# Kernel optimization log

Hardware: AMD Instinct MI355X
Metric: run time of the kernel (lower is better)

## Reference

```python
import jax, jax.numpy as jnp
import numpy as np

B, T, M, S = 16384, 128, 4, 12  # num_series, timesteps, measurements, states


def setup_inputs() -> dict:
    key = jax.random.key(0)
    ks = jax.random.split(key, 7)
    inp = jax.random.normal(ks[0], (B, T, M), dtype=jnp.float32)
    # stable transition matrix near identity
    F = jnp.eye(S, dtype=jnp.float32) + 0.05 * jax.random.normal(ks[1], (S, S), dtype=jnp.float32) / np.float32(np.sqrt(S))
    H = jax.random.normal(ks[2], (M, S), dtype=jnp.float32) / np.float32(np.sqrt(S))
    Aq = 0.1 * jax.random.normal(ks[3], (S, S), dtype=jnp.float32)
    Q = Aq @ Aq.T + 1e-3 * jnp.eye(S, dtype=jnp.float32)  # PSD process noise
    Ar = 0.1 * jax.random.normal(ks[4], (M, M), dtype=jnp.float32)
    R = Ar @ Ar.T + 1e-3 * jnp.eye(M, dtype=jnp.float32)  # PSD measurement noise
    m0 = jax.random.normal(ks[5], (B, S, 1), dtype=jnp.float32)
    Ap = 0.1 * jax.random.normal(ks[6], (B, S, S), dtype=jnp.float32)
    P0 = jnp.einsum('bij,bkj->bik', Ap, Ap) + 1e-2 * jnp.eye(S, dtype=jnp.float32)
    return {"inp": inp, "F": F, "H": H, "Q": Q, "R": R, "m0": m0, "P0": P0}


def _kalman_forward(inp, F, H, Q, R, m0, P0):
    I_S = jnp.eye(S, dtype=inp.dtype)
    # t = -1 step of the original loop: one predict from the initial state
    m = jnp.einsum('ij,bjk->bik', F, m0)                      # [B,S,1]
    P = jnp.einsum('ij,bjk,lk->bil', F, P0, F) + Q            # [B,S,S]

    def step(carry, obs_t):
        m, P = carry  # one-step-ahead prior at time t
        y = jnp.einsum('ms,bsk->bmk', H, m)                   # predicted measurement [B,M,1]
        # --- kf_update ---
        resid = obs_t - y[..., 0]                             # [B,M]
        Sm = jnp.einsum('ms,bst,nt->bmn', H, P, H) + R        # innovation cov [B,M,M]
        Sinv = jnp.linalg.inv(Sm)
        K = jnp.einsum('bst,mt,bmn->bsn', P, H, Sinv)         # Kalman gain [B,S,M]
        m_f = m + jnp.einsum('bsm,bm->bs', K, resid)[..., None]
        ImKH = I_S - jnp.einsum('bsm,mt->bst', K, H)
        # Joseph stabilized covariance update
        P_f = (jnp.einsum('bij,bjk,blk->bil', ImKH, P, ImKH)
               + jnp.einsum('bim,mn,bjn->bij', K, R, K))
        # --- kf_predict for next timestep ---
        m_n = jnp.einsum('ij,bjk->bik', F, m_f)
        P_n = jnp.einsum('ij,bjk,lk->bil', F, P_f, F) + Q
        return (m_n, P_n), y

    _, ys = jax.lax.scan(step, (m, P), jnp.swapaxes(inp, 0, 1))  # ys: [T,B,M,1]
    # original forward does torch.cat(predicted_measurements, 0) -> [T*B, M, 1]
    return ys.reshape(T * B, M, 1)


def reference(inp, F, H, Q, R, m0, P0):
    return _kalman_forward(inp, F, H, Q, R, m0, P0)
```

## Files before the change

kernel.cpp:

```cpp
#include <hip/hip_runtime.h>

#define BN 16384
#define TT 128
#define MM 4
#define SS 12
#define BLOCK 64
#define NSER (BLOCK / 4)
#define TSTRIDE 145


template<int CTRL>
__device__ __forceinline__ float dpp32(float v) {
    union { int i; float f; } u, o;
    u.f = v;
    o.i = __builtin_amdgcn_update_dpp(0, u.i, CTRL, 0xF, 0xF, true);
    return o.f;
}
template<int CTRL>
__device__ __forceinline__ double dpp64(double v) {
    union { double d; int i[2]; } u, o;
    u.d = v;
    o.i[0] = __builtin_amdgcn_update_dpp(0, u.i[0], CTRL, 0xF, 0xF, true);
    o.i[1] = __builtin_amdgcn_update_dpp(0, u.i[1], CTRL, 0xF, 0xF, true);
    return o.d;
}
__device__ __forceinline__ double qsum(double v) {
    v += dpp64<0xB1>(v);
    v += dpp64<0x4E>(v);
    return v;
}

__global__ __launch_bounds__(BLOCK, 1) void kf_kernel(
    const float* __restrict__ inp,
    const float* __restrict__ Fm,
    const float* __restrict__ Hm,
    const float* __restrict__ Qm,
    const float* __restrict__ Rm,
    const float* __restrict__ m0p,
    const float* __restrict__ P0p,
    float* __restrict__ outp)
{
    __shared__ double Fd[SS * SS];
    __shared__ double Hd[MM * SS];
    __shared__ double Qd[SS * SS];
    __shared__ double Rd[MM * MM];
    __shared__ double tb[NSER * TSTRIDE];

    const int tid  = threadIdx.x;
    const int gid  = blockIdx.x * BLOCK + tid;
    const int b    = gid >> 2;
    const int c    = gid & 3;
    const int sb   = tid >> 2;
    const int col0 = 3 * c;

    for (int i = tid; i < SS * SS; i += BLOCK) {
        Fd[i] = (double)Fm[i];
        Qd[i] = (double)Qm[i];
    }
    if (tid < MM * SS) Hd[tid] = (double)Hm[tid];
    if (tid < MM * MM) Rd[tid] = (double)Rm[tid];

    double m[SS];
#pragma unroll
    for (int s = 0; s < SS; ++s) m[s] = (double)m0p[b * SS + s];

    double P[SS][3];
#pragma unroll
    for (int s = 0; s < SS; ++s)
#pragma unroll
        for (int jj = 0; jj < 3; ++jj)
            P[s][jj] = (double)P0p[b * SS * SS + s * SS + col0 + jj];

    const float* op = inp + b * (TT * MM) + c;
    float obn = op[0];
    double* tser = &tb[sb * TSTRIDE];

    __syncthreads();

#pragma unroll 1
    for (int t = 0; t < TT; ++t) {
        __builtin_amdgcn_wave_barrier();
#pragma unroll
        for (int i = 0; i < SS; ++i) {
            double fr[SS];
#pragma unroll
            for (int s = 0; s < SS; ++s) fr[s] = Fd[i * SS + s];
            double u0 = 0.0, u1 = 0.0, u2 = 0.0;
#pragma unroll
            for (int s = 0; s < SS; ++s) {
                u0 += fr[s] * P[s][0];
                u1 += fr[s] * P[s][1];
                u2 += fr[s] * P[s][2];
            }
            tser[i * SS + col0 + 0] = u0;
            tser[i * SS + col0 + 1] = u1;
            tser[i * SS + col0 + 2] = u2;
        }

        double mvl[3];
#pragma unroll
        for (int jj = 0; jj < 3; ++jj) {
            double a = 0.0;
#pragma unroll
            for (int s = 0; s < SS; ++s) a += Fd[(col0 + jj) * SS + s] * m[s];
            mvl[jj] = a;
        }

        __builtin_amdgcn_wave_barrier();

#pragma unroll
        for (int h = 0; h < 2; ++h) {
            double Ur[3][6];
#pragma unroll
            for (int jj = 0; jj < 3; ++jj)
#pragma unroll
                for (int kk = 0; kk < 6; ++kk)
                    Ur[jj][kk] = tser[(col0 + jj) * SS + h * 6 + kk];
#pragma unroll
            for (int s = 0; s < SS; ++s) {
                double fr6[6];
#pragma unroll
                for (int kk = 0; kk < 6; ++kk) fr6[kk] = Fd[s * SS + h * 6 + kk];
                double p0 = (h == 0) ? Qd[s * SS + col0 + 0] : P[s][0];
                double p1 = (h == 0) ? Qd[s * SS + col0 + 1] : P[s][1];
                double p2 = (h == 0) ? Qd[s * SS + col0 + 2] : P[s][2];
#pragma unroll
                for (int kk = 0; kk < 6; ++kk) {
                    p0 += Ur[0][kk] * fr6[kk];
                    p1 += Ur[1][kk] * fr6[kk];
                    p2 += Ur[2][kk] * fr6[kk];
                }
                P[s][0] = p0; P[s][1] = p1; P[s][2] = p2;
            }
        }

        double y[MM];
#pragma unroll
        for (int n = 0; n < MM; ++n) {
            double py = Hd[n * SS + col0 + 0] * mvl[0]
                      + Hd[n * SS + col0 + 1] * mvl[1]
                      + Hd[n * SS + col0 + 2] * mvl[2];
            y[n] = qsum(py);
        }
        double ysel = (c & 2) ? ((c & 1) ? y[3] : y[2]) : ((c & 1) ? y[1] : y[0]);
        outp[t * (BN * MM) + b * MM + c] = (float)ysel;

        float obc = obn;
        if (t + 1 < TT) obn = op[(t + 1) * MM];

        double r[MM];
        r[0] = (double)dpp32<0x00>(obc) - y[0];
        r[1] = (double)dpp32<0x55>(obc) - y[1];
        r[2] = (double)dpp32<0xAA>(obc) - y[2];
        r[3] = (double)dpp32<0xFF>(obc) - y[3];

        double HPl[MM][3];
#pragma unroll
        for (int n = 0; n < MM; ++n) {
            double h0 = 0.0, h1 = 0.0, h2 = 0.0;
#pragma unroll
            for (int s = 0; s < SS; ++s) {
                double hv = Hd[n * SS + s];
                h0 += hv * P[s][0]; h1 += hv * P[s][1]; h2 += hv * P[s][2];
            }
            HPl[n][0] = h0; HPl[n][1] = h1; HPl[n][2] = h2;
        }

        double Su[10];
        {
            int u = 0;
#pragma unroll
            for (int n = 0; n < MM; ++n)
#pragma unroll
                for (int t2 = 0; t2 < MM; ++t2) {
                    if (t2 < n) continue;
                    double acc = HPl[n][0] * Hd[t2 * SS + col0 + 0]
                               + HPl[n][1] * Hd[t2 * SS + col0 + 1]
                               + HPl[n][2] * Hd[t2 * SS + col0 + 2];
                    Su[u] = qsum(acc) + Rd[n * MM + t2];
                    ++u;
                }
        }
        double s00 = Su[0], s01 = Su[1], s02 = Su[2], s03 = Su[3];
        double s11 = Su[4], s12 = Su[5], s13 = Su[6];
        double s22 = Su[7], s23 = Su[8], s33 = Su[9];

        double ra   = 1.0 / (s00 * s11 - s01 * s01);
        double ai00 = s11 * ra, ai01 = -s01 * ra, ai11 = s00 * ra;
        double w00 = ai00 * s02 + ai01 * s12;
        double w01 = ai00 * s03 + ai01 * s13;
        double w10 = ai01 * s02 + ai11 * s12;
        double w11 = ai01 * s03 + ai11 * s13;
        double e00 = s22 - (s02 * w00 + s12 * w10);
        double e01 = s23 - (s02 * w01 + s12 * w11);
        double e11 = s33 - (s03 * w01 + s13 * w11);
        double rmm = 1.0 / (e00 * e11 - e01 * e01);
        double q22 = e11 * rmm, q23 = -e01 * rmm, q33 = e00 * rmm;
        double x00 = w00 * q22 + w01 * q23;
        double x01 = w00 * q23 + w01 * q33;
        double x10 = w10 * q22 + w11 * q23;
        double x11 = w10 * q23 + w11 * q33;
        double q00 = ai00 + x00 * w00 + x01 * w01;
        double q01 = ai01 + x00 * w10 + x01 * w11;
        double q11 = ai11 + x10 * w10 + x11 * w11;
        double Qi[MM][MM] = {
            { q00,  q01,  -x00, -x01 },
            { q01,  q11,  -x10, -x11 },
            { -x00, -x10,  q22,  q23 },
            { -x01, -x11,  q23,  q33 }
        };

        double z0 = Qi[0][0] * r[0] + Qi[0][1] * r[1] + Qi[0][2] * r[2] + Qi[0][3] * r[3];
        double z1 = Qi[1][0] * r[0] + Qi[1][1] * r[1] + Qi[1][2] * r[2] + Qi[1][3] * r[3];
        double z2 = Qi[2][0] * r[0] + Qi[2][1] * r[1] + Qi[2][2] * r[2] + Qi[2][3] * r[3];
        double z3 = Qi[3][0] * r[0] + Qi[3][1] * r[1] + Qi[3][2] * r[2] + Qi[3][3] * r[3];

        double pm[3];
#pragma unroll
        for (int jj = 0; jj < 3; ++jj)
            pm[jj] = mvl[jj] + HPl[0][jj] * z0 + HPl[1][jj] * z1
                   + HPl[2][jj] * z2 + HPl[3][jj] * z3;

        m[0]  = dpp64<0x00>(pm[0]);  m[1]  = dpp64<0x00>(pm[1]);  m[2]  = dpp64<0x00>(pm[2]);
        m[3]  = dpp64<0x55>(pm[0]);  m[4]  = dpp64<0x55>(pm[1]);  m[5]  = dpp64<0x55>(pm[2]);
        m[6]  = dpp64<0xAA>(pm[0]);  m[7]  = dpp64<0xAA>(pm[1]);  m[8]  = dpp64<0xAA>(pm[2]);
        m[9]  = dpp64<0xFF>(pm[0]);  m[10] = dpp64<0xFF>(pm[1]);  m[11] = dpp64<0xFF>(pm[2]);

        double G[MM][3];
#pragma unroll
        for (int n = 0; n < MM; ++n)
#pragma unroll
            for (int jj = 0; jj < 3; ++jj)
                G[n][jj] = Qi[n][0] * HPl[0][jj] + Qi[n][1] * HPl[1][jj]
                         + Qi[n][2] * HPl[2][jj] + Qi[n][3] * HPl[3][jj];

#pragma unroll
        for (int jr = 0; jr < 3; ++jr) {
            {
                double h0 = dpp64<0x00>(HPl[0][jr]), h1 = dpp64<0x00>(HPl[1][jr]);
                double h2 = dpp64<0x00>(HPl[2][jr]), h3 = dpp64<0x00>(HPl[3][jr]);
#pragma unroll
                for (int jj = 0; jj < 3; ++jj)
                    P[jr][jj] -= h0 * G[0][jj] + h1 * G[1][jj] + h2 * G[2][jj] + h3 * G[3][jj];
            }
            {
                double h0 = dpp64<0x55>(HPl[0][jr]), h1 = dpp64<0x55>(HPl[1][jr]);
                double h2 = dpp64<0x55>(HPl[2][jr]), h3 = dpp64<0x55>(HPl[3][jr]);
#pragma unroll
                for (int jj = 0; jj < 3; ++jj)
                    P[3 + jr][jj] -= h0 * G[0][jj] + h1 * G[1][jj] + h2 * G[2][jj] + h3 * G[3][jj];
            }
            {
                double h0 = dpp64<0xAA>(HPl[0][jr]), h1 = dpp64<0xAA>(HPl[1][jr]);
                double h2 = dpp64<0xAA>(HPl[2][jr]), h3 = dpp64<0xAA>(HPl[3][jr]);
#pragma unroll
                for (int jj = 0; jj < 3; ++jj)
                    P[6 + jr][jj] -= h0 * G[0][jj] + h1 * G[1][jj] + h2 * G[2][jj] + h3 * G[3][jj];
            }
            {
                double h0 = dpp64<0xFF>(HPl[0][jr]), h1 = dpp64<0xFF>(HPl[1][jr]);
                double h2 = dpp64<0xFF>(HPl[2][jr]), h3 = dpp64<0xFF>(HPl[3][jr]);
#pragma unroll
                for (int jj = 0; jj < 3; ++jj)
                    P[9 + jr][jj] -= h0 * G[0][jj] + h1 * G[1][jj] + h2 * G[2][jj] + h3 * G[3][jj];
            }
        }
    }
}

extern "C" void kernel_launch(void* const* d_in, const int* in_sizes, int n_in,
                              void* d_out, int out_size, void* d_ws, size_t ws_size,
                              hipStream_t stream) {
    const float* inp = (const float*)d_in[0];
    const float* F   = (const float*)d_in[1];
    const float* H   = (const float*)d_in[2];
    const float* Q   = (const float*)d_in[3];
    const float* R   = (const float*)d_in[4];
    const float* m0  = (const float*)d_in[5];
    const float* P0  = (const float*)d_in[6];
    float* out = (float*)d_out;

    dim3 grid((BN * MM) / BLOCK), block(BLOCK);
    hipLaunchKernelGGL(kf_kernel, grid, block, 0, stream,
                       inp, F, H, Q, R, m0, P0, out);
}
```

Before: 792.3 us.

## Reorder Kalman recurrence so predict overlaps innovation inverse via F-propagated gain terms

Peels the first predict out of the time loop and restructures each step so the covariance predict (F P F^T + Q) of the prior is computed before the rank-4 update, with the update propagated through F (V = F·PH^T) instead of applied before the predict. This moves the F-sandwich off the critical path after the 4x4 inverse, letting the LDS-bound predict overlap the innovation computation. It adds extra DPP shuffles and FLOPs for computing V and requires the algebraic identity F(P - K S K^T)F^T = FPF^T - V S^-1 V^T to hold, which may change rounding slightly.

```diff
diff --git a/kernel.cpp b/kernel.cpp
--- a/kernel.cpp
+++ b/kernel.cpp
@@ -60,16 +60,16 @@
     if (tid < MM * SS) Hd[tid] = (double)Hm[tid];
     if (tid < MM * MM) Rd[tid] = (double)Rm[tid];
 
-    double m[SS];
-#pragma unroll
-    for (int s = 0; s < SS; ++s) m[s] = (double)m0p[b * SS + s];
-
     double P[SS][3];
 #pragma unroll
     for (int s = 0; s < SS; ++s)
 #pragma unroll
         for (int jj = 0; jj < 3; ++jj)
             P[s][jj] = (double)P0p[b * SS * SS + s * SS + col0 + jj];
+
+    double mtmp[SS];
+#pragma unroll
+    for (int s = 0; s < SS; ++s) mtmp[s] = (double)m0p[b * SS + s];
 
     const float* op = inp + b * (TT * MM) + c;
     float obn = op[0];
@@ -77,9 +77,66 @@
 
     __syncthreads();
 
+#pragma unroll
+    for (int i = 0; i < SS; ++i) {
+        double fr[SS];
+#pragma unroll
+        for (int s = 0; s < SS; ++s) fr[s] = Fd[i * SS + s];
+        double u0 = 0.0, u1 = 0.0, u2 = 0.0;
+#pragma unroll
+        for (int s = 0; s < SS; ++s) {
+            u0 += fr[s] * P[s][0];
+            u1 += fr[s] * P[s][1];
+            u2 += fr[s] * P[s][2];
+        }
+        tser[i * SS + col0 + 0] = u0;
+        tser[i * SS + col0 + 1] = u1;
+        tser[i * SS + col0 + 2] = u2;
+    }
+    double pmv[3];
+#pragma unroll
+    for (int jj = 0; jj < 3; ++jj) {
+        double a = 0.0;
+#pragma unroll
+        for (int s = 0; s < SS; ++s) a += Fd[(col0 + jj) * SS + s] * mtmp[s];
+        pmv[jj] = a;
+    }
+    __builtin_amdgcn_wave_barrier();
+#pragma unroll
+    for (int h = 0; h < 2; ++h) {
+        double Ur[3][6];
+#pragma unroll
+        for (int jj = 0; jj < 3; ++jj)
+#pragma unroll
+            for (int kk = 0; kk < 6; ++kk)
+                Ur[jj][kk] = tser[(col0 + jj) * SS + h * 6 + kk];
+#pragma unroll
+        for (int s = 0; s < SS; ++s) {
+            double fr6[6];
+#pragma unroll
+            for (int kk = 0; kk < 6; ++kk) fr6[kk] = Fd[s * SS + h * 6 + kk];
+            double p0 = (h == 0) ? Qd[s * SS + col0 + 0] : P[s][0];
+            double p1 = (h == 0) ? Qd[s * SS + col0 + 1] : P[s][1];
+            double p2 = (h == 0) ? Qd[s * SS + col0 + 2] : P[s][2];
+#pragma unroll
+            for (int kk = 0; kk < 6; ++kk) {
+                p0 += Ur[0][kk] * fr6[kk];
+                p1 += Ur[1][kk] * fr6[kk];
+                p2 += Ur[2][kk] * fr6[kk];
+            }
+            P[s][0] = p0; P[s][1] = p1; P[s][2] = p2;
+        }
+    }
+    double mvf[SS];
+    mvf[0]  = dpp64<0x00>(pmv[0]);  mvf[1]  = dpp64<0x00>(pmv[1]);  mvf[2]  = dpp64<0x00>(pmv[2]);
+    mvf[3]  = dpp64<0x55>(pmv[0]);  mvf[4]  = dpp64<0x55>(pmv[1]);  mvf[5]  = dpp64<0x55>(pmv[2]);
+    mvf[6]  = dpp64<0xAA>(pmv[0]);  mvf[7]  = dpp64<0xAA>(pmv[1]);  mvf[8]  = dpp64<0xAA>(pmv[2]);
+    mvf[9]  = dpp64<0xFF>(pmv[0]);  mvf[10] = dpp64<0xFF>(pmv[1]);  mvf[11] = dpp64<0xFF>(pmv[2]);
+
 #pragma unroll 1
     for (int t = 0; t < TT; ++t) {
         __builtin_amdgcn_wave_barrier();
+
 #pragma unroll
         for (int i = 0; i < SS; ++i) {
             double fr[SS];
@@ -97,49 +154,21 @@
             tser[i * SS + col0 + 2] = u2;
         }
 
-        double mvl[3];
+        double fmv[3];
 #pragma unroll
         for (int jj = 0; jj < 3; ++jj) {
             double a = 0.0;
 #pragma unroll
-            for (int s = 0; s < SS; ++s) a += Fd[(col0 + jj) * SS + s] * m[s];
-            mvl[jj] = a;
-        }
-
-        __builtin_amdgcn_wave_barrier();
-
-#pragma unroll
-        for (int h = 0; h < 2; ++h) {
-            double Ur[3][6];
-#pragma unroll
-            for (int jj = 0; jj < 3; ++jj)
-#pragma unroll
-                for (int kk = 0; kk < 6; ++kk)
-                    Ur[jj][kk] = tser[(col0 + jj) * SS + h * 6 + kk];
-#pragma unroll
-            for (int s = 0; s < SS; ++s) {
-                double fr6[6];
-#pragma unroll
-                for (int kk = 0; kk < 6; ++kk) fr6[kk] = Fd[s * SS + h * 6 + kk];
-                double p0 = (h == 0) ? Qd[s * SS + col0 + 0] : P[s][0];
-                double p1 = (h == 0) ? Qd[s * SS + col0 + 1] : P[s][1];
-                double p2 = (h == 0) ? Qd[s * SS + col0 + 2] : P[s][2];
-#pragma unroll
-                for (int kk = 0; kk < 6; ++kk) {
-                    p0 += Ur[0][kk] * fr6[kk];
-                    p1 += Ur[1][kk] * fr6[kk];
-                    p2 += Ur[2][kk] * fr6[kk];
-                }
-                P[s][0] = p0; P[s][1] = p1; P[s][2] = p2;
-            }
+            for (int s = 0; s < SS; ++s) a += Fd[(col0 + jj) * SS + s] * mvf[s];
+            fmv[jj] = a;
         }
 
         double y[MM];
 #pragma unroll
         for (int n = 0; n < MM; ++n) {
-            double py = Hd[n * SS + col0 + 0] * mvl[0]
-                      + Hd[n * SS + col0 + 1] * mvl[1]
-                      + Hd[n * SS + col0 + 2] * mvl[2];
+            double py = Hd[n * SS + col0 + 0] * mvf[col0 + 0]
+                      + Hd[n * SS + col0 + 1] * mvf[col0 + 1]
+                      + Hd[n * SS + col0 + 2] * mvf[col0 + 2];
             y[n] = qsum(py);
         }
         double ysel = (c & 2) ? ((c & 1) ? y[3] : y[2]) : ((c & 1) ? y[1] : y[0]);
@@ -184,6 +213,92 @@
         double s00 = Su[0], s01 = Su[1], s02 = Su[2], s03 = Su[3];
         double s11 = Su[4], s12 = Su[5], s13 = Su[6];
         double s22 = Su[7], s23 = Su[8], s33 = Su[9];
+
+        __builtin_amdgcn_wave_barrier();
+
+#pragma unroll
+        for (int h = 0; h < 2; ++h) {
+            double Ur[3][6];
+#pragma unroll
+            for (int jj = 0; jj < 3; ++jj)
+#pragma unroll
+                for (int kk = 0; kk < 6; ++kk)
+                    Ur[jj][kk] = tser[(col0 + jj) * SS + h * 6 + kk];
+#pragma unroll
+            for (int s = 0; s < SS; ++s) {
+                double fr6[6];
+#pragma unroll
+                for (int kk = 0; kk < 6; ++kk) fr6[kk] = Fd[s * SS + h * 6 + kk];
+                double p0 = (h == 0) ? Qd[s * SS + col0 + 0] : P[s][0];
+                double p1 = (h == 0) ? Qd[s * SS + col0 + 1] : P[s][1];
+                double p2 = (h == 0) ? Qd[s * SS + col0 + 2] : P[s][2];
+#pragma unroll
+                for (int kk = 0; kk < 6; ++kk) {
+                    p0 += Ur[0][kk] * fr6[kk];
+                    p1 += Ur[1][kk] * fr6[kk];
+                    p2 += Ur[2][kk] * fr6[kk];
+                }
+                P[s][0] = p0; P[s][1] = p1; P[s][2] = p2;
+            }
+        }
+
+        double Vl[MM][3];
+        {
+            double h00 = dpp64<0x00>(HPl[0][0]), h01 = dpp64<0x00>(HPl[0][1]), h02 = dpp64<0x00>(HPl[0][2]);
+            double h10 = dpp64<0x00>(HPl[1][0]), h11 = dpp64<0x00>(HPl[1][1]), h12 = dpp64<0x00>(HPl[1][2]);
+            double h20 = dpp64<0x00>(HPl[2][0]), h21 = dpp64<0x00>(HPl[2][1]), h22 = dpp64<0x00>(HPl[2][2]);
+            double h30 = dpp64<0x00>(HPl[3][0]), h31 = dpp64<0x00>(HPl[3][1]), h32 = dpp64<0x00>(HPl[3][2]);
+#pragma unroll
+            for (int jj = 0; jj < 3; ++jj) {
+                double f0 = Fd[(col0 + jj) * SS + 0], f1 = Fd[(col0 + jj) * SS + 1], f2 = Fd[(col0 + jj) * SS + 2];
+                Vl[0][jj] = h00 * f0 + h01 * f1 + h02 * f2;
+                Vl[1][jj] = h10 * f0 + h11 * f1 + h12 * f2;
+                Vl[2][jj] = h20 * f0 + h21 * f1 + h22 * f2;
+                Vl[3][jj] = h30 * f0 + h31 * f1 + h32 * f2;
+            }
+        }
+        {
+            double h00 = dpp64<0x55>(HPl[0][0]), h01 = dpp64<0x55>(HPl[0][1]), h02 = dpp64<0x55>(HPl[0][2]);
+            double h10 = dpp64<0x55>(HPl[1][0]), h11 = dpp64<0x55>(HPl[1][1]), h12 = dpp64<0x55>(HPl[1][2]);
+            double h20 = dpp64<0x55>(HPl[2][0]), h21 = dpp64<0x55>(HPl[2][1]), h22 = dpp64<0x55>(HPl[2][2]);
+            double h30 = dpp64<0x55>(HPl[3][0]), h31 = dpp64<0x55>(HPl[3][1]), h32 = dpp64<0x55>(HPl[3][2]);
+#pragma unroll
+            for (int jj = 0; jj < 3; ++jj) {
+                double f0 = Fd[(col0 + jj) * SS + 3], f1 = Fd[(col0 + jj) * SS + 4], f2 = Fd[(col0 + jj) * SS + 5];
+                Vl[0][jj] += h00 * f0 + h01 * f1 + h02 * f2;
+                Vl[1][jj] += h10 * f0 + h11 * f1 + h12 * f2;
+                Vl[2][jj] += h20 * f0 + h21 * f1 + h22 * f2;
+                Vl[3][jj] += h30 * f0 + h31 * f1 + h32 * f2;
+            }
+        }
+        {
+            double h00 = dpp64<0xAA>(HPl[0][0]), h01 = dpp64<0xAA>(HPl[0][1]), h02 = dpp64<0xAA>(HPl[0][2]);
+            double h10 = dpp64<0xAA>(HPl[1][0]), h11 = dpp64<0xAA>(HPl[1][1]), h12 = dpp64<0xAA>(HPl[1][2]);
+            double h20 = dpp64<0xAA>(HPl[2][0]), h21 = dpp64<0xAA>(HPl[2][1]), h22 = dpp64<0xAA>(HPl[2][2]);
+            double h30 = dpp64<0xAA>(HPl[3][0]), h31 = dpp64<0xAA>(HPl[3][1]), h32 = dpp64<0xAA>(HPl[3][2]);
+#pragma unroll
+            for (int jj = 0; jj < 3; ++jj) {
+                double f0 = Fd[(col0 + jj) * SS + 6], f1 = Fd[(col0 + jj) * SS + 7], f2 = Fd[(col0 + jj) * SS + 8];
+                Vl[0][jj] += h00 * f0 + h01 * f1 + h02 * f2;
+                Vl[1][jj] += h10 * f0 + h11 * f1 + h12 * f2;
+                Vl[2][jj] += h20 * f0 + h21 * f1 + h22 * f2;
+                Vl[3][jj] += h30 * f0 + h31 * f1 + h32 * f2;
+            }
+        }
+        {
+            double h00 = dpp64<0xFF>(HPl[0][0]), h01 = dpp64<0xFF>(HPl[0][1]), h02 = dpp64<0xFF>(HPl[0][2]);
+            double h10 = dpp64<0xFF>(HPl[1][0]), h11 = dpp64<0xFF>(HPl[1][1]), h12 = dpp64<0xFF>(HPl[1][2]);
+            double h20 = dpp64<0xFF>(HPl[2][0]), h21 = dpp64<0xFF>(HPl[2][1]), h22 = dpp64<0xFF>(HPl[2][2]);
+            double h30 = dpp64<0xFF>(HPl[3][0]), h31 = dpp64<0xFF>(HPl[3][1]), h32 = dpp64<0xFF>(HPl[3][2]);
+#pragma unroll
+            for (int jj = 0; jj < 3; ++jj) {
+                double f0 = Fd[(col0 + jj) * SS + 9], f1 = Fd[(col0 + jj) * SS + 10], f2 = Fd[(col0 + jj) * SS + 11];
+                Vl[0][jj] += h00 * f0 + h01 * f1 + h02 * f2;
+                Vl[1][jj] += h10 * f0 + h11 * f1 + h12 * f2;
+                Vl[2][jj] += h20 * f0 + h21 * f1 + h22 * f2;
+                Vl[3][jj] += h30 * f0 + h31 * f1 + h32 * f2;
+            }
+        }
 
         double ra   = 1.0 / (s00 * s11 - s01 * s01);
         double ai00 = s11 * ra, ai01 = -s01 * ra, ai11 = s00 * ra;
@@ -215,56 +330,73 @@
         double z2 = Qi[2][0] * r[0] + Qi[2][1] * r[1] + Qi[2][2] * r[2] + Qi[2][3] * r[3];
         double z3 = Qi[3][0] * r[0] + Qi[3][1] * r[1] + Qi[3][2] * r[2] + Qi[3][3] * r[3];
 
-        double pm[3];
+        double G2[MM][3];
+#pragma unroll
+        for (int n = 0; n < MM; ++n)
+#pragma unroll
+            for (int jj = 0; jj < 3; ++jj)
+                G2[n][jj] = Qi[n][0] * Vl[0][jj] + Qi[n][1] * Vl[1][jj]
+                          + Qi[n][2] * Vl[2][jj] + Qi[n][3] * Vl[3][jj];
+
+        {
+            double v00 = dpp64<0x00>(Vl[0][0]), v01 = dpp64<0x00>(Vl[0][1]), v02 = dpp64<0x00>(Vl[0][2]);
+            double v10 = dpp64<0x00>(Vl[1][0]), v11 = dpp64<0x00>(Vl[1][1]), v12 = dpp64<0x00>(Vl[1][2]);
+            double v20 = dpp64<0x00>(Vl[2][0]), v21 = dpp64<0x00>(Vl[2][1]), v22 = dpp64<0x00>(Vl[2][2]);
+            double v30 = dpp64<0x00>(Vl[3][0]), v31 = dpp64<0x00>(Vl[3][1]), v32 = dpp64<0x00>(Vl[3][2]);
+#pragma unroll
+            for (int jj = 0; jj < 3; ++jj) {
+                P[0][jj] -= v00 * G2[0][jj] + v10 * G2[1][jj] + v20 * G2[2][jj] + v30 * G2[3][jj];
+                P[1][jj] -= v01 * G2[0][jj] + v11 * G2[1][jj] + v21 * G2[2][jj] + v31 * G2[3][jj];
+                P[2][jj] -= v02 * G2[0][jj] + v12 * G2[1][jj] + v22 * G2[2][jj] + v32 * G2[3][jj];
+            }
+        }
+        {
+            double v00 = dpp64<0x55>(Vl[0][0]), v01 = dpp64<0x55>(Vl[0][1]), v02 = dpp64<0x55>(Vl[0][2]);
+            double v10 = dpp64<0x55>(Vl[1][0]), v11 = dpp64<0x55>(Vl[1][1]), v12 = dpp64<0x55>(Vl[1][2]);
+            double v20 = dpp64<0x55>(Vl[2][0]), v21 = dpp64<0x55>(Vl[2][1]), v22 = dpp64<0x55>(Vl[2][2]);
+            double v30 = dpp64<0x55>(Vl[3][0]), v31 = dpp64<0x55>(Vl[3][1]), v32 = dpp64<0x55>(Vl[3][2]);
+#pragma unroll
+            for (int jj = 0; jj < 3; ++jj) {
+                P[3][jj] -= v00 * G2[0][jj] + v10 * G2[1][jj] + v20 * G2[2][jj] + v30 * G2[3][jj];
+                P[4][jj] -= v01 * G2[0][jj] + v11 * G2[1][jj] + v21 * G2[2][jj] + v31 * G2[3][jj];
+                P[5][jj] -= v02 * G2[0][jj] + v12 * G2[1][jj] + v22 * G2[2][jj] + v32 * G2[3][jj];
+            }
+        }
+        {
+            double v00 = dpp64<0xAA>(Vl[0][0]), v01 = dpp64<0xAA>(Vl[0][1]), v02 = dpp64<0xAA>(Vl[0][2]);
+            double v10 = dpp64<0xAA>(Vl[1][0]), v11 = dpp64<0xAA>(Vl[1][1]), v12 = dpp64<0xAA>(Vl[1][2]);
+            double v20 = dpp64<0xAA>(Vl[2][0]), v21 = dpp64<0xAA>(Vl[2][1]), v22 = dpp64<0xAA>(Vl[2][2]);
+            double v30 = dpp64<0xAA>(Vl[3][0]), v31 = dpp64<0xAA>(Vl[3][1]), v32 = dpp64<0xAA>(Vl[3][2]);
+#pragma unroll
+            for (int jj = 0; jj < 3; ++jj) {
+                P[6][jj] -= v00 * G2[0][jj] + v10 * G2[1][jj] + v20 * G2[2][jj] + v30 * G2[3][jj];
+                P[7][jj] -= v01 * G2[0][jj] + v11 * G2[1][jj] + v21 * G2[2][jj] + v31 * G2[3][jj];
+                P[8][jj] -= v02 * G2[0][jj] + v12 * G2[1][jj] + v22 * G2[2][jj] + v32 * G2[3][jj];
+            }
+        }
+        {
+            double v00 = dpp64<0xFF>(Vl[0][0]), v01 = dpp64<0xFF>(Vl[0][1]), v02 = dpp64<0xFF>(Vl[0][2]);
+            double v10 = dpp64<0xFF>(Vl[1][0]), v11 = dpp64<0xFF>(Vl[1][1]), v12 = dpp64<0xFF>(Vl[1][2]);
+            double v20 = dpp64<0xFF>(Vl[2][0]), v21 = dpp64<0xFF>(Vl[2][1]), v22 = dpp64<0xFF>(Vl[2][2]);
+            double v30 = dpp64<0xFF>(Vl[3][0]), v31 = dpp64<0xFF>(Vl[3][1]), v32 = dpp64<0xFF>(Vl[3][2]);
+#pragma unroll
+            for (int jj = 0; jj < 3; ++jj) {
+                P[9][jj]  -= v00 * G2[0][jj] + v10 * G2[1][jj] + v20 * G2[2][jj] + v30 * G2[3][jj];
+                P[10][jj] -= v01 * G2[0][jj] + v11 * G2[1][jj] + v21 * G2[2][jj] + v31 * G2[3][jj];
+                P[11][jj] -= v02 * G2[0][jj] + v12 * G2[1][jj] + v22 * G2[2][jj] + v32 * G2[3][jj];
+            }
+        }
+
+        double mvn[3];
 #pragma unroll
         for (int jj = 0; jj < 3; ++jj)
-            pm[jj] = mvl[jj] + HPl[0][jj] * z0 + HPl[1][jj] * z1
-                   + HPl[2][jj] * z2 + HPl[3][jj] * z3;
-
-        m[0]  = dpp64<0x00>(pm[0]);  m[1]  = dpp64<0x00>(pm[1]);  m[2]  = dpp64<0x00>(pm[2]);
-        m[3]  = dpp64<0x55>(pm[0]);  m[4]  = dpp64<0x55>(pm[1]);  m[5]  = dpp64<0x55>(pm[2]);
-        m[6]  = dpp64<0xAA>(pm[0]);  m[7]  = dpp64<0xAA>(pm[1]);  m[8]  = dpp64<0xAA>(pm[2]);
-        m[9]  = dpp64<0xFF>(pm[0]);  m[10] = dpp64<0xFF>(pm[1]);  m[11] = dpp64<0xFF>(pm[2]);
-
-        double G[MM][3];
-#pragma unroll
-        for (int n = 0; n < MM; ++n)
-#pragma unroll
-            for (int jj = 0; jj < 3; ++jj)
-                G[n][jj] = Qi[n][0] * HPl[0][jj] + Qi[n][1] * HPl[1][jj]
-                         + Qi[n][2] * HPl[2][jj] + Qi[n][3] * HPl[3][jj];
-
-#pragma unroll
-        for (int jr = 0; jr < 3; ++jr) {
-            {
-                double h0 = dpp64<0x00>(HPl[0][jr]), h1 = dpp64<0x00>(HPl[1][jr]);
-                double h2 = dpp64<0x00>(HPl[2][jr]), h3 = dpp64<0x00>(HPl[3][jr]);
-#pragma unroll
-                for (int jj = 0; jj < 3; ++jj)
-                    P[jr][jj] -= h0 * G[0][jj] + h1 * G[1][jj] + h2 * G[2][jj] + h3 * G[3][jj];
-            }
-            {
-                double h0 = dpp64<0x55>(HPl[0][jr]), h1 = dpp64<0x55>(HPl[1][jr]);
-                double h2 = dpp64<0x55>(HPl[2][jr]), h3 = dpp64<0x55>(HPl[3][jr]);
-#pragma unroll
-                for (int jj = 0; jj < 3; ++jj)
-                    P[3 + jr][jj] -= h0 * G[0][jj] + h1 * G[1][jj] + h2 * G[2][jj] + h3 * G[3][jj];
-            }
-            {
-                double h0 = dpp64<0xAA>(HPl[0][jr]), h1 = dpp64<0xAA>(HPl[1][jr]);
-                double h2 = dpp64<0xAA>(HPl[2][jr]), h3 = dpp64<0xAA>(HPl[3][jr]);
-#pragma unroll
-                for (int jj = 0; jj < 3; ++jj)
-                    P[6 + jr][jj] -= h0 * G[0][jj] + h1 * G[1][jj] + h2 * G[2][jj] + h3 * G[3][jj];
-            }
-            {
-                double h0 = dpp64<0xFF>(HPl[0][jr]), h1 = dpp64<0xFF>(HPl[1][jr]);
-                double h2 = dpp64<0xFF>(HPl[2][jr]), h3 = dpp64<0xFF>(HPl[3][jr]);
-#pragma unroll
-                for (int jj = 0; jj < 3; ++jj)
-                    P[9 + jr][jj] -= h0 * G[0][jj] + h1 * G[1][jj] + h2 * G[2][jj] + h3 * G[3][jj];
-            }
-        }
+            mvn[jj] = fmv[jj] + Vl[0][jj] * z0 + Vl[1][jj] * z1
+                    + Vl[2][jj] * z2 + Vl[3][jj] * z3;
+
+        mvf[0]  = dpp64<0x00>(mvn[0]);  mvf[1]  = dpp64<0x00>(mvn[1]);  mvf[2]  = dpp64<0x00>(mvn[2]);
+        mvf[3]  = dpp64<0x55>(mvn[0]);  mvf[4]  = dpp64<0x55>(mvn[1]);  mvf[5]  = dpp64<0x55>(mvn[2]);
+        mvf[6]  = dpp64<0xAA>(mvn[0]);  mvf[7]  = dpp64<0xAA>(mvn[1]);  mvf[8]  = dpp64<0xAA>(mvn[2]);
+        mvf[9]  = dpp64<0xFF>(mvn[0]);  mvf[10] = dpp64<0xFF>(mvn[1]);  mvf[11] = dpp64<0xFF>(mvn[2]);
     }
 }
 
```

Measured after the change: 849.1 us. 7.2% more time.

## Split each series across 8 lanes and replace LDS transpose with swizzle/DPP

Applied to the files above, without the earlier changes.

Each Kalman series is now handled by 8 lanes instead of 4: each lane owns a 6x3 tile of the covariance, halving per-lane registers and FLOPs. The F*P*F^T predict no longer goes through a shared-memory transpose buffer; the partial products are combined across the two halves with ds_swizzle and broadcast within quads with DPP. Launch bounds change to allow 2 waves per block-slot, and the grid doubles. This adds cross-lane traffic, duplicates the scalar innovation/inverse work across both halves, and doubles the thread count.

```diff
diff --git a/kernel.cpp b/kernel.cpp
--- a/kernel.cpp
+++ b/kernel.cpp
@@ -5,8 +5,6 @@
 #define MM 4
 #define SS 12
 #define BLOCK 64
-#define NSER (BLOCK / 4)
-#define TSTRIDE 145
 
 
 template<int CTRL>
@@ -29,8 +27,15 @@
     v += dpp64<0x4E>(v);
     return v;
 }
-
-__global__ __launch_bounds__(BLOCK, 1) void kf_kernel(
+__device__ __forceinline__ double swz4(double v) {
+    union { double d; int i[2]; } u, o;
+    u.d = v;
+    o.i[0] = __builtin_amdgcn_ds_swizzle(u.i[0], 0x101F);
+    o.i[1] = __builtin_amdgcn_ds_swizzle(u.i[1], 0x101F);
+    return o.d;
+}
+
+__global__ __launch_bounds__(BLOCK, 2) void kf_kernel(
     const float* __restrict__ inp,
     const float* __restrict__ Fm,
     const float* __restrict__ Hm,
@@ -44,14 +49,16 @@
     __shared__ double Hd[MM * SS];
     __shared__ double Qd[SS * SS];
     __shared__ double Rd[MM * MM];
-    __shared__ double tb[NSER * TSTRIDE];
-
-    const int tid  = threadIdx.x;
-    const int gid  = blockIdx.x * BLOCK + tid;
-    const int b    = gid >> 2;
-    const int c    = gid & 3;
-    const int sb   = tid >> 2;
-    const int col0 = 3 * c;
+
+    const int tid   = threadIdx.x;
+    const int gid   = blockIdx.x * BLOCK + tid;
+    const int b     = gid >> 3;
+    const int d     = tid & 7;
+    const int h     = d >> 2;
+    const int c     = d & 3;
+    const int col0  = 3 * c;
+    const int hrow0 = 6 * h;
+    const int orow0 = 6 - hrow0;
 
     for (int i = tid; i < SS * SS; i += BLOCK) {
         Fd[i] = (double)Fm[i];
@@ -60,42 +67,46 @@
     if (tid < MM * SS) Hd[tid] = (double)Hm[tid];
     if (tid < MM * MM) Rd[tid] = (double)Rm[tid];
 
+    double P[6][3];
+#pragma unroll
+    for (int ii = 0; ii < 6; ++ii)
+#pragma unroll
+        for (int jj = 0; jj < 3; ++jj)
+            P[ii][jj] = (double)P0p[b * SS * SS + (hrow0 + ii) * SS + col0 + jj];
+
     double m[SS];
 #pragma unroll
     for (int s = 0; s < SS; ++s) m[s] = (double)m0p[b * SS + s];
-
-    double P[SS][3];
-#pragma unroll
-    for (int s = 0; s < SS; ++s)
-#pragma unroll
-        for (int jj = 0; jj < 3; ++jj)
-            P[s][jj] = (double)P0p[b * SS * SS + s * SS + col0 + jj];
 
     const float* op = inp + b * (TT * MM) + c;
     float obn = op[0];
-    double* tser = &tb[sb * TSTRIDE];
 
     __syncthreads();
 
 #pragma unroll 1
     for (int t = 0; t < TT; ++t) {
-        __builtin_amdgcn_wave_barrier();
-#pragma unroll
-        for (int i = 0; i < SS; ++i) {
-            double fr[SS];
-#pragma unroll
-            for (int s = 0; s < SS; ++s) fr[s] = Fd[i * SS + s];
-            double u0 = 0.0, u1 = 0.0, u2 = 0.0;
-#pragma unroll
-            for (int s = 0; s < SS; ++s) {
-                u0 += fr[s] * P[s][0];
-                u1 += fr[s] * P[s][1];
-                u2 += fr[s] * P[s][2];
+        double pOwn[6][3], pOth[6][3];
+#pragma unroll
+        for (int ii = 0; ii < 6; ++ii) {
+#pragma unroll
+            for (int jj = 0; jj < 3; ++jj) { pOwn[ii][jj] = 0.0; pOth[ii][jj] = 0.0; }
+#pragma unroll
+            for (int s = 0; s < 6; ++s) {
+                double fo = Fd[(hrow0 + ii) * SS + hrow0 + s];
+                double ft = Fd[(orow0 + ii) * SS + hrow0 + s];
+#pragma unroll
+                for (int jj = 0; jj < 3; ++jj) {
+                    pOwn[ii][jj] += fo * P[s][jj];
+                    pOth[ii][jj] += ft * P[s][jj];
+                }
             }
-            tser[i * SS + col0 + 0] = u0;
-            tser[i * SS + col0 + 1] = u1;
-            tser[i * SS + col0 + 2] = u2;
-        }
+        }
+        double U[6][3];
+#pragma unroll
+        for (int ii = 0; ii < 6; ++ii)
+#pragma unroll
+            for (int jj = 0; jj < 3; ++jj)
+                U[ii][jj] = pOwn[ii][jj] + swz4(pOth[ii][jj]);
 
         double mvl[3];
 #pragma unroll
@@ -106,32 +117,83 @@
             mvl[jj] = a;
         }
 
-        __builtin_amdgcn_wave_barrier();
-
-#pragma unroll
-        for (int h = 0; h < 2; ++h) {
-            double Ur[3][6];
-#pragma unroll
-            for (int jj = 0; jj < 3; ++jj)
-#pragma unroll
-                for (int kk = 0; kk < 6; ++kk)
-                    Ur[jj][kk] = tser[(col0 + jj) * SS + h * 6 + kk];
-#pragma unroll
-            for (int s = 0; s < SS; ++s) {
-                double fr6[6];
-#pragma unroll
-                for (int kk = 0; kk < 6; ++kk) fr6[kk] = Fd[s * SS + h * 6 + kk];
-                double p0 = (h == 0) ? Qd[s * SS + col0 + 0] : P[s][0];
-                double p1 = (h == 0) ? Qd[s * SS + col0 + 1] : P[s][1];
-                double p2 = (h == 0) ? Qd[s * SS + col0 + 2] : P[s][2];
-#pragma unroll
-                for (int kk = 0; kk < 6; ++kk) {
-                    p0 += Ur[0][kk] * fr6[kk];
-                    p1 += Ur[1][kk] * fr6[kk];
-                    p2 += Ur[2][kk] * fr6[kk];
-                }
-                P[s][0] = p0; P[s][1] = p1; P[s][2] = p2;
-            }
+#pragma unroll
+        for (int ii = 0; ii < 6; ++ii)
+#pragma unroll
+            for (int jj = 0; jj < 3; ++jj)
+                P[ii][jj] = Qd[(hrow0 + ii) * SS + col0 + jj];
+
+        {
+            double Uq[6][3];
+#pragma unroll
+            for (int ii = 0; ii < 6; ++ii)
+#pragma unroll
+                for (int kk = 0; kk < 3; ++kk) Uq[ii][kk] = dpp64<0x00>(U[ii][kk]);
+            double fq[3][3];
+#pragma unroll
+            for (int jj = 0; jj < 3; ++jj)
+#pragma unroll
+                for (int kk = 0; kk < 3; ++kk) fq[jj][kk] = Fd[(col0 + jj) * SS + 0 + kk];
+#pragma unroll
+            for (int ii = 0; ii < 6; ++ii)
+#pragma unroll
+                for (int jj = 0; jj < 3; ++jj)
+#pragma unroll
+                    for (int kk = 0; kk < 3; ++kk) P[ii][jj] += Uq[ii][kk] * fq[jj][kk];
+        }
+        {
+            double Uq[6][3];
+#pragma unroll
+            for (int ii = 0; ii < 6; ++ii)
+#pragma unroll
+                for (int kk = 0; kk < 3; ++kk) Uq[ii][kk] = dpp64<0x55>(U[ii][kk]);
+            double fq[3][3];
+#pragma unroll
+            for (int jj = 0; jj < 3; ++jj)
+#pragma unroll
+                for (int kk = 0; kk < 3; ++kk) fq[jj][kk] = Fd[(col0 + jj) * SS + 3 + kk];
+#pragma unroll
+            for (int ii = 0; ii < 6; ++ii)
+#pragma unroll
+                for (int jj = 0; jj < 3; ++jj)
+#pragma unroll
+                    for (int kk = 0; kk < 3; ++kk) P[ii][jj] += Uq[ii][kk] * fq[jj][kk];
+        }
+        {
+            double Uq[6][3];
+#pragma unroll
+            for (int ii = 0; ii < 6; ++ii)
+#pragma unroll
+                for (int kk = 0; kk < 3; ++kk) Uq[ii][kk] = dpp64<0xAA>(U[ii][kk]);
+            double fq[3][3];
+#pragma unroll
+            for (int jj = 0; jj < 3; ++jj)
+#pragma unroll
+                for (int kk = 0; kk < 3; ++kk) fq[jj][kk] = Fd[(col0 + jj) * SS + 6 + kk];
+#pragma unroll
+            for (int ii = 0; ii < 6; ++ii)
+#pragma unroll
+                for (int jj = 0; jj < 3; ++jj)
+#pragma unroll
+                    for (int kk = 0; kk < 3; ++kk) P[ii][jj] += Uq[ii][kk] * fq[jj][kk];
+        }
+        {
+            double Uq[6][3];
+#pragma unroll
+            for (int ii = 0; ii < 6; ++ii)
+#pragma unroll
+                for (int kk = 0; kk < 3; ++kk) Uq[ii][kk] = dpp64<0xFF>(U[ii][kk]);
+            double fq[3][3];
+#pragma unroll
+            for (int jj = 0; jj < 3; ++jj)
+#pragma unroll
+                for (int kk = 0; kk < 3; ++kk) fq[jj][kk] = Fd[(col0 + jj) * SS + 9 + kk];
+#pragma unroll
+            for (int ii = 0; ii < 6; ++ii)
+#pragma unroll
+                for (int jj = 0; jj < 3; ++jj)
+#pragma unroll
+                    for (int kk = 0; kk < 3; ++kk) P[ii][jj] += Uq[ii][kk] * fq[jj][kk];
         }
 
         double y[MM];
@@ -143,27 +205,28 @@
             y[n] = qsum(py);
         }
         double ysel = (c & 2) ? ((c & 1) ? y[3] : y[2]) : ((c & 1) ? y[1] : y[0]);
-        outp[t * (BN * MM) + b * MM + c] = (float)ysel;
+        if (h == 0) outp[t * (BN * MM) + b * MM + c] = (float)ysel;
 
         float obc = obn;
         if (t + 1 < TT) obn = op[(t + 1) * MM];
 
-        double r[MM];
-        r[0] = (double)dpp32<0x00>(obc) - y[0];
-        r[1] = (double)dpp32<0x55>(obc) - y[1];
-        r[2] = (double)dpp32<0xAA>(obc) - y[2];
-        r[3] = (double)dpp32<0xFF>(obc) - y[3];
+        double r0v = (double)dpp32<0x00>(obc) - y[0];
+        double r1v = (double)dpp32<0x55>(obc) - y[1];
+        double r2v = (double)dpp32<0xAA>(obc) - y[2];
+        double r3v = (double)dpp32<0xFF>(obc) - y[3];
 
         double HPl[MM][3];
 #pragma unroll
         for (int n = 0; n < MM; ++n) {
             double h0 = 0.0, h1 = 0.0, h2 = 0.0;
 #pragma unroll
-            for (int s = 0; s < SS; ++s) {
-                double hv = Hd[n * SS + s];
+            for (int s = 0; s < 6; ++s) {
+                double hv = Hd[n * SS + hrow0 + s];
                 h0 += hv * P[s][0]; h1 += hv * P[s][1]; h2 += hv * P[s][2];
             }
-            HPl[n][0] = h0; HPl[n][1] = h1; HPl[n][2] = h2;
+            HPl[n][0] = h0 + swz4(h0);
+            HPl[n][1] = h1 + swz4(h1);
+            HPl[n][2] = h2 + swz4(h2);
         }
 
         double Su[10];
@@ -210,10 +273,10 @@
             { -x01, -x11,  q23,  q33 }
         };
 
-        double z0 = Qi[0][0] * r[0] + Qi[0][1] * r[1] + Qi[0][2] * r[2] + Qi[0][3] * r[3];
-        double z1 = Qi[1][0] * r[0] + Qi[1][1] * r[1] + Qi[1][2] * r[2] + Qi[1][3] * r[3];
-        double z2 = Qi[2][0] * r[0] + Qi[2][1] * r[1] + Qi[2][2] * r[2] + Qi[2][3] * r[3];
-        double z3 = Qi[3][0] * r[0] + Qi[3][1] * r[1] + Qi[3][2] * r[2] + Qi[3][3] * r[3];
+        double z0 = Qi[0][0] * r0v + Qi[0][1] * r1v + Qi[0][2] * r2v + Qi[0][3] * r3v;
+        double z1 = Qi[1][0] * r0v + Qi[1][1] * r1v + Qi[1][2] * r2v + Qi[1][3] * r3v;
+        double z2 = Qi[2][0] * r0v + Qi[2][1] * r1v + Qi[2][2] * r2v + Qi[2][3] * r3v;
+        double z3 = Qi[3][0] * r0v + Qi[3][1] * r1v + Qi[3][2] * r2v + Qi[3][3] * r3v;
 
         double pm[3];
 #pragma unroll
@@ -234,36 +297,49 @@
                 G[n][jj] = Qi[n][0] * HPl[0][jj] + Qi[n][1] * HPl[1][jj]
                          + Qi[n][2] * HPl[2][jj] + Qi[n][3] * HPl[3][jj];
 
-#pragma unroll
-        for (int jr = 0; jr < 3; ++jr) {
-            {
-                double h0 = dpp64<0x00>(HPl[0][jr]), h1 = dpp64<0x00>(HPl[1][jr]);
-                double h2 = dpp64<0x00>(HPl[2][jr]), h3 = dpp64<0x00>(HPl[3][jr]);
-#pragma unroll
-                for (int jj = 0; jj < 3; ++jj)
-                    P[jr][jj] -= h0 * G[0][jj] + h1 * G[1][jj] + h2 * G[2][jj] + h3 * G[3][jj];
-            }
-            {
-                double h0 = dpp64<0x55>(HPl[0][jr]), h1 = dpp64<0x55>(HPl[1][jr]);
-                double h2 = dpp64<0x55>(HPl[2][jr]), h3 = dpp64<0x55>(HPl[3][jr]);
-#pragma unroll
-                for (int jj = 0; jj < 3; ++jj)
-                    P[3 + jr][jj] -= h0 * G[0][jj] + h1 * G[1][jj] + h2 * G[2][jj] + h3 * G[3][jj];
-            }
-            {
-                double h0 = dpp64<0xAA>(HPl[0][jr]), h1 = dpp64<0xAA>(HPl[1][jr]);
-                double h2 = dpp64<0xAA>(HPl[2][jr]), h3 = dpp64<0xAA>(HPl[3][jr]);
-#pragma unroll
-                for (int jj = 0; jj < 3; ++jj)
-                    P[6 + jr][jj] -= h0 * G[0][jj] + h1 * G[1][jj] + h2 * G[2][jj] + h3 * G[3][jj];
-            }
-            {
-                double h0 = dpp64<0xFF>(HPl[0][jr]), h1 = dpp64<0xFF>(HPl[1][jr]);
-                double h2 = dpp64<0xFF>(HPl[2][jr]), h3 = dpp64<0xFF>(HPl[3][jr]);
-#pragma unroll
-                for (int jj = 0; jj < 3; ++jj)
-                    P[9 + jr][jj] -= h0 * G[0][jj] + h1 * G[1][jj] + h2 * G[2][jj] + h3 * G[3][jj];
-            }
+        {
+            double b0[MM][3], b2[MM][3];
+#pragma unroll
+            for (int n = 0; n < MM; ++n)
+#pragma unroll
+                for (int jj = 0; jj < 3; ++jj) {
+                    b0[n][jj] = dpp64<0x00>(HPl[n][jj]);
+                    b2[n][jj] = dpp64<0xAA>(HPl[n][jj]);
+                }
+            double bs[MM][3];
+#pragma unroll
+            for (int n = 0; n < MM; ++n)
+#pragma unroll
+                for (int ii = 0; ii < 3; ++ii)
+                    bs[n][ii] = h ? b2[n][ii] : b0[n][ii];
+#pragma unroll
+            for (int ii = 0; ii < 3; ++ii)
+#pragma unroll
+                for (int jj = 0; jj < 3; ++jj)
+                    P[ii][jj] -= bs[0][ii] * G[0][jj] + bs[1][ii] * G[1][jj]
+                               + bs[2][ii] * G[2][jj] + bs[3][ii] * G[3][jj];
+        }
+        {
+            double b1[MM][3], b3[MM][3];
+#pragma unroll
+            for (int n = 0; n < MM; ++n)
+#pragma unroll
+                for (int jj = 0; jj < 3; ++jj) {
+                    b1[n][jj] = dpp64<0x55>(HPl[n][jj]);
+                    b3[n][jj] = dpp64<0xFF>(HPl[n][jj]);
+                }
+            double bs[MM][3];
+#pragma unroll
+            for (int n = 0; n < MM; ++n)
+#pragma unroll
+                for (int ii = 0; ii < 3; ++ii)
+                    bs[n][ii] = h ? b3[n][ii] : b1[n][ii];
+#pragma unroll
+            for (int ii = 0; ii < 3; ++ii)
+#pragma unroll
+                for (int jj = 0; jj < 3; ++jj)
+                    P[3 + ii][jj] -= bs[0][ii] * G[0][jj] + bs[1][ii] * G[1][jj]
+                                   + bs[2][ii] * G[2][jj] + bs[3][ii] * G[3][jj];
         }
     }
 }
@@ -280,7 +356,7 @@
     const float* P0  = (const float*)d_in[6];
     float* out = (float*)d_out;
 
-    dim3 grid((BN * MM) / BLOCK), block(BLOCK);
+    dim3 grid((BN * 8) / BLOCK), block(BLOCK);
     hipLaunchKernelGGL(kf_kernel, grid, block, 0, stream,
                        inp, F, H, Q, R, m0, P0, out);
 }
```

Result: slower. 3.134 ms (+295.6%).
